# Kernel optimization log

Hardware: AMD Instinct MI355X
Metric: run time of the kernel (lower is better)

The kernel has to match this reference:

```python
import jax, jax.numpy as jnp
import numpy as np

THRESH = 0.85

def setup_inputs() -> dict:
    key = jax.random.key(0)
    k1, k2 = jax.random.split(key)
    bs, d, r, c = 4, 16, 64, 64
    n = r * c
    seg = jax.random.normal(k1, (bs, d, r, c), dtype=jnp.float32)
    W = jax.random.uniform(k2, (bs, n, n), dtype=jnp.float32)
    return {"seg": seg, "W": W}

def reference(seg, W):
    bs, d, r, c = seg.shape
    # threshold affinity: keep values > 0.85
    Wt = jnp.where(W > THRESH, W, jnp.zeros((), W.dtype))
    # row-normalize: D = diag(1/rowsum(Wt)) @ Wt  (broadcast division)
    D = Wt / Wt.sum(axis=-1, keepdims=True)          # [bs, n, n]
    seg_flat = seg.reshape(bs, d, r * c)             # [bs, d, n]
    # seg_flat @ D^T : out[b,d,m] = sum_n seg[b,d,n] * D[b,m,n]
    out = jnp.einsum('bdn,bmn->bdm', seg_flat, D)
    return out.reshape(bs, d, r, c)
```

## Files before the change

### kernel.cpp

```cpp
#include <hip/hip_runtime.h>
#include <stdint.h>


typedef float v4f __attribute__((ext_vector_type(4)));

#define N_DIM 4096
#define D_DIM 16
#define THRESH 0.85f
#define RPW 4
#define CHUNK 256
#define NCHUNK (N_DIM / CHUNK)

__global__ __launch_bounds__(256) void regu_kernel(
    const float* __restrict__ seg,
    const float* __restrict__ W,
    float* __restrict__ out)
{
    __shared__ float stile[2][D_DIM * CHUNK];

    const int lane = threadIdx.x & 63;
    const int wv   = threadIdx.x >> 6;
    const int row0 = blockIdx.x * 16 + wv * RPW;
    const int b  = row0 >> 12;
    const int m0 = row0 & (N_DIM - 1);

    const float* Wp   = W   + ((size_t)b * N_DIM + m0) * N_DIM + lane * 4;
    const float* segb = seg + (size_t)b * D_DIM * N_DIM;

    float acc[RPW * D_DIM];
    float rowsum[RPW] = {0.f, 0.f, 0.f, 0.f};
#pragma unroll
    for (int i = 0; i < RPW * D_DIM; ++i) acc[i] = 0.f;

#define STAGE(c, sb)                                                          \
    do {                                                                      \
        _Pragma("unroll")                                                     \
        for (int j = 0; j < 4; ++j) {                                         \
            const int d_ = wv * 4 + j;                                        \
            const float* g_ = segb + (size_t)d_ * N_DIM + (c) * CHUNK + lane * 4; \
            __builtin_amdgcn_global_load_lds(                                 \
                (const __attribute__((address_space(1))) uint32_t*)g_,        \
                (__attribute__((address_space(3))) uint32_t*)&stile[sb][d_ * CHUNK], \
                16, 0, 0);                                                    \
        }                                                                     \
    } while (0)

    v4f wA[RPW], wB[RPW];

    STAGE(0, 0);
#pragma unroll
    for (int r = 0; r < RPW; ++r)
        wA[r] = __builtin_nontemporal_load((const v4f*)(Wp + (size_t)r * N_DIM));
    __syncthreads();

    auto compute = [&](const v4f* w_in, int sb) {
        v4f w[RPW];
#pragma unroll
        for (int r = 0; r < RPW; ++r) {
            v4f v = w_in[r];
            v.x = (v.x > THRESH) ? v.x : 0.f;
            v.y = (v.y > THRESH) ? v.y : 0.f;
            v.z = (v.z > THRESH) ? v.z : 0.f;
            v.w = (v.w > THRESH) ? v.w : 0.f;
            w[r] = v;
            rowsum[r] += (v.x + v.y) + (v.z + v.w);
        }
#pragma unroll
        for (int d = 0; d < D_DIM; ++d) {
            const v4f s = *(const v4f*)&stile[sb][d * CHUNK + lane * 4];
#pragma unroll
            for (int r = 0; r < RPW; ++r) {
                acc[r * D_DIM + d] += w[r].x * s.x;
                acc[r * D_DIM + d] += w[r].y * s.y;
                acc[r * D_DIM + d] += w[r].z * s.z;
                acc[r * D_DIM + d] += w[r].w * s.w;
            }
        }
    };

    for (int c = 0; c < NCHUNK; c += 2) {
        STAGE(c + 1, 1);
        {
            const float* p = Wp + (size_t)(c + 1) * CHUNK;
#pragma unroll
            for (int r = 0; r < RPW; ++r)
                wB[r] = __builtin_nontemporal_load((const v4f*)(p + (size_t)r * N_DIM));
        }
        compute(wA, 0);
        __syncthreads();

        if (c + 2 < NCHUNK) {
            STAGE(c + 2, 0);
            const float* p = Wp + (size_t)(c + 2) * CHUNK;
#pragma unroll
            for (int r = 0; r < RPW; ++r)
                wA[r] = __builtin_nontemporal_load((const v4f*)(p + (size_t)r * N_DIM));
        }
        compute(wB, 1);
        __syncthreads();
    }

#pragma unroll
    for (int k = 0; k < 6; ++k) {
        const int S = 32 >> k;
        const bool up = (lane >> k) & 1;
#pragma unroll
        for (int j = 0; j < S; ++j) {
            const float mine = up ? acc[j + S] : acc[j];
            const float send = up ? acc[j] : acc[j + S];
            acc[j] = mine + __shfl_xor(send, 1 << k, 64);
        }
    }

#pragma unroll
    for (int r = 0; r < RPW; ++r) {
        float s = rowsum[r];
#pragma unroll
        for (int off = 1; off < 64; off <<= 1) s += __shfl_xor(s, off, 64);
        rowsum[r] = s;
    }

    const int j = __brev((unsigned)lane) >> 26;
    const int r = j >> 4;
    const int d = j & 15;
    const float inv = 1.0f / (r < 2 ? (r == 0 ? rowsum[0] : rowsum[1])
                                    : (r == 2 ? rowsum[2] : rowsum[3]));
    out[((size_t)b * D_DIM + d) * N_DIM + (m0 + r)] = acc[0] * inv;
}

extern "C" void kernel_launch(void* const* d_in, const int* in_sizes, int n_in,
                              void* d_out, int out_size, void* d_ws, size_t ws_size,
                              hipStream_t stream) {
    const float* seg = (const float*)d_in[0];
    const float* W   = (const float*)d_in[1];
    float* out = (float*)d_out;

    regu_kernel<<<1024, 256, 0, stream>>>(seg, W, out);
}
```

Measured before the change: 354.3 us.

## Replace LDS-staged seg tiles with direct register loads and drop barriers

Removes the shared-memory double buffer for seg and its block-wide __syncthreads, loading seg vectors straight from global (L2-cached) into registers with a 4-row software prefetch pipeline. The W prefetch for the next chunk is moved to the last group of the current chunk. It also adds an occupancy hint of 4 blocks per CU to the launch bounds. The trade is that seg is now read from cache by every wave instead of once per block through LDS, and register pressure rises from the extra prefetch buffers.

```diff
diff --git a/kernel.cpp b/kernel.cpp
--- a/kernel.cpp
+++ b/kernel.cpp
@@ -1,5 +1,4 @@
 #include <hip/hip_runtime.h>
-#include <stdint.h>
 
 
 typedef float v4f __attribute__((ext_vector_type(4)));
@@ -11,13 +10,11 @@
 #define CHUNK 256
 #define NCHUNK (N_DIM / CHUNK)
 
-__global__ __launch_bounds__(256) void regu_kernel(
+__global__ __launch_bounds__(256, 4) void regu_kernel(
     const float* __restrict__ seg,
     const float* __restrict__ W,
     float* __restrict__ out)
 {
-    __shared__ float stile[2][D_DIM * CHUNK];
-
     const int lane = threadIdx.x & 63;
     const int wv   = threadIdx.x >> 6;
     const int row0 = blockIdx.x * 16 + wv * RPW;
@@ -25,79 +22,70 @@
     const int m0 = row0 & (N_DIM - 1);
 
     const float* Wp   = W   + ((size_t)b * N_DIM + m0) * N_DIM + lane * 4;
-    const float* segb = seg + (size_t)b * D_DIM * N_DIM;
+    const float* segp = seg + (size_t)b * D_DIM * N_DIM + lane * 4;
 
     float acc[RPW * D_DIM];
     float rowsum[RPW] = {0.f, 0.f, 0.f, 0.f};
 #pragma unroll
     for (int i = 0; i < RPW * D_DIM; ++i) acc[i] = 0.f;
 
-#define STAGE(c, sb)                                                          \
-    do {                                                                      \
-        _Pragma("unroll")                                                     \
-        for (int j = 0; j < 4; ++j) {                                         \
-            const int d_ = wv * 4 + j;                                        \
-            const float* g_ = segb + (size_t)d_ * N_DIM + (c) * CHUNK + lane * 4; \
-            __builtin_amdgcn_global_load_lds(                                 \
-                (const __attribute__((address_space(1))) uint32_t*)g_,        \
-                (__attribute__((address_space(3))) uint32_t*)&stile[sb][d_ * CHUNK], \
-                16, 0, 0);                                                    \
-        }                                                                     \
-    } while (0)
-
     v4f wA[RPW], wB[RPW];
 
-    STAGE(0, 0);
 #pragma unroll
     for (int r = 0; r < RPW; ++r)
         wA[r] = __builtin_nontemporal_load((const v4f*)(Wp + (size_t)r * N_DIM));
-    __syncthreads();
 
-    auto compute = [&](const v4f* w_in, int sb) {
-        v4f w[RPW];
+    auto body = [&](v4f* wcur, v4f* wnext, int c, bool prefetch) {
+        const float* sp = segp + c * CHUNK;
+        v4f s[4];
+
+#pragma unroll
+        for (int q = 0; q < 4; ++q)
+            s[q] = *(const v4f*)(sp + q * N_DIM);
+
 #pragma unroll
         for (int r = 0; r < RPW; ++r) {
-            v4f v = w_in[r];
+            v4f v = wcur[r];
             v.x = (v.x > THRESH) ? v.x : 0.f;
             v.y = (v.y > THRESH) ? v.y : 0.f;
             v.z = (v.z > THRESH) ? v.z : 0.f;
             v.w = (v.w > THRESH) ? v.w : 0.f;
-            w[r] = v;
+            wcur[r] = v;
             rowsum[r] += (v.x + v.y) + (v.z + v.w);
         }
+
 #pragma unroll
-        for (int d = 0; d < D_DIM; ++d) {
-            const v4f s = *(const v4f*)&stile[sb][d * CHUNK + lane * 4];
+        for (int g = 0; g < 4; ++g) {
+            v4f snext[4];
+            if (g < 3) {
 #pragma unroll
-            for (int r = 0; r < RPW; ++r) {
-                acc[r * D_DIM + d] += w[r].x * s.x;
-                acc[r * D_DIM + d] += w[r].y * s.y;
-                acc[r * D_DIM + d] += w[r].z * s.z;
-                acc[r * D_DIM + d] += w[r].w * s.w;
+                for (int q = 0; q < 4; ++q)
+                    snext[q] = *(const v4f*)(sp + ((g + 1) * 4 + q) * N_DIM);
+            } else if (prefetch) {
+#pragma unroll
+                for (int r = 0; r < RPW; ++r)
+                    wnext[r] = __builtin_nontemporal_load(
+                        (const v4f*)(Wp + (size_t)(c + 1) * CHUNK + (size_t)r * N_DIM));
             }
+#pragma unroll
+            for (int q = 0; q < 4; ++q) {
+                const int d = g * 4 + q;
+#pragma unroll
+                for (int r = 0; r < RPW; ++r) {
+                    acc[r * D_DIM + d] += wcur[r].x * s[q].x;
+                    acc[r * D_DIM + d] += wcur[r].y * s[q].y;
+                    acc[r * D_DIM + d] += wcur[r].z * s[q].z;
+                    acc[r * D_DIM + d] += wcur[r].w * s[q].w;
+                }
+            }
+#pragma unroll
+            for (int q = 0; q < 4; ++q) s[q] = snext[q];
         }
     };
 
     for (int c = 0; c < NCHUNK; c += 2) {
-        STAGE(c + 1, 1);
-        {
-            const float* p = Wp + (size_t)(c + 1) * CHUNK;
-#pragma unroll
-            for (int r = 0; r < RPW; ++r)
-                wB[r] = __builtin_nontemporal_load((const v4f*)(p + (size_t)r * N_DIM));
-        }
-        compute(wA, 0);
-        __syncthreads();
-
-        if (c + 2 < NCHUNK) {
-            STAGE(c + 2, 0);
-            const float* p = Wp + (size_t)(c + 2) * CHUNK;
-#pragma unroll
-            for (int r = 0; r < RPW; ++r)
-                wA[r] = __builtin_nontemporal_load((const v4f*)(p + (size_t)r * N_DIM));
-        }
-        compute(wB, 1);
-        __syncthreads();
+        body(wA, wB, c, true);
+        body(wB, wA, c + 1, c + 2 < NCHUNK);
     }
 
 #pragma unroll
```

New measurement: 767.5 us. +116.6%, slower.
